# Optimization experiments

Measured on AMD Instinct MI355X. Metric: run time of the kernel, lower is better.

Reference implementation:

```python
import jax, jax.numpy as jnp
import numpy as np

EMBED_DIM = 96
OUT_DIM = 192
HEADS = 2
HEAD_DIM = OUT_DIM // HEADS  # 96
STRIDE_Q = (1, 2, 2)
STRIDE_KV = (1, 8, 8)
SCALE = 1.0 / float(np.sqrt(HEAD_DIM))


def layer_norm(x, g, b, eps=1e-5):
    m = jnp.mean(x, -1, keepdims=True)
    v = jnp.mean(jnp.square(x - m), -1, keepdims=True)
    return (x - m) * jax.lax.rsqrt(v + eps) * g + b


def pool(x, thw, conv_w, g, b, stride):
    # x: [B, heads, N, d] with cls token at position 0; depthwise conv3d pool + LayerNorm(d)
    B, nh, N, d = x.shape
    T, H, W = thw
    cls_tok, rest = x[:, :, :1], x[:, :, 1:]
    rest = rest.transpose(0, 1, 3, 2).reshape(B * nh, d, T, H, W)
    rest = jax.lax.conv_general_dilated(
        rest, conv_w, stride, [(1, 1), (1, 1), (1, 1)],
        dimension_numbers=('NCDHW', 'OIDHW', 'NCDHW'), feature_group_count=d)
    T2, H2, W2 = rest.shape[2], rest.shape[3], rest.shape[4]
    rest = rest.reshape(B, nh, d, -1).transpose(0, 1, 3, 2)
    x = jnp.concatenate([cls_tok, rest], axis=2)
    return layer_norm(x, g, b), (T2, H2, W2)


def rel_idx(q_n, k_n):
    # decomposed relative-distance indices with q/k resolution ratio scaling
    q_r = max(k_n / q_n, 1.0)
    k_r = max(q_n / k_n, 1.0)
    d = (jnp.arange(q_n, dtype=jnp.float32)[:, None] * q_r
         - jnp.arange(k_n, dtype=jnp.float32)[None, :] * k_r + (k_n - 1) * k_r)
    return d.astype(jnp.int32)


def add_rel_pos(attn, q, q_thw, k_thw, rph, rpw, rpt):
    qt, qh, qw = q_thw
    kt, kh, kw = k_thw
    Rh = rph[rel_idx(qh, kh)]  # [qh, kh, d]
    Rw = rpw[rel_idx(qw, kw)]  # [qw, kw, d]
    Rt = rpt[rel_idx(qt, kt)]  # [qt, kt, d]
    B, nh, qN, d = q.shape
    r_q = q[:, :, 1:].reshape(B, nh, qt, qh, qw, d)
    rel_h = jnp.einsum('bythwc,hkc->bythwk', r_q, Rh)  # k = kh
    rel_w = jnp.einsum('bythwc,wkc->bythwk', r_q, Rw)  # k = kw
    rel_t = jnp.einsum('bythwc,tkc->bythwk', r_q, Rt)  # k = kt
    rel = (rel_t[..., :, None, None] + rel_h[..., None, :, None]
           + rel_w[..., None, None, :]).reshape(B, nh, qt * qh * qw, kt * kh * kw)
    return attn.at[:, :, 1:, 1:].add(rel)


def _forward(x, qkv_w, qkv_b, proj_w, proj_b, pq_w, nq_g, nq_b, pk_w, nk_g, nk_b,
             pv_w, nv_g, nv_b, rel_pos_h, rel_pos_w, rel_pos_t, thw):
    B, N, C = x.shape
    qkv = (x @ qkv_w.T + qkv_b).reshape(B, N, 3, HEADS, HEAD_DIM).transpose(2, 0, 3, 1, 4)
    q, k, v = qkv[0], qkv[1], qkv[2]  # each [B, heads, N, head_dim]
    k, k_thw = pool(k, thw, pk_w, nk_g, nk_b, STRIDE_KV)
    v, _ = pool(v, thw, pv_w, nv_g, nv_b, STRIDE_KV)
    q, q_thw = pool(q, thw, pq_w, nq_g, nq_b, STRIDE_Q)
    attn = jnp.einsum('bhqd,bhkd->bhqk', q * SCALE, k)
    attn = add_rel_pos(attn, q, q_thw, k_thw, rel_pos_h, rel_pos_w, rel_pos_t)
    attn = jax.nn.softmax(attn, axis=-1)
    out = jnp.einsum('bhqk,bhkd->bhqd', attn, v) + q  # residual_pool, with cls embed
    out = out.transpose(0, 2, 1, 3).reshape(B, -1, OUT_DIM)
    return out @ proj_w.T + proj_b


def setup_inputs() -> dict:
    key = jax.random.key(0)
    ks = jax.random.split(key, 10)
    T, H, W = 8, 56, 56
    N = 1 + T * H * W  # 25089
    B = 4
    std = 0.02
    return {
        'x': jax.random.normal(ks[0], (B, N, EMBED_DIM), jnp.float32),
        'qkv_w': jax.random.normal(ks[1], (3 * OUT_DIM, EMBED_DIM), jnp.float32) * std,
        'qkv_b': jnp.zeros((3 * OUT_DIM,), jnp.float32),
        'proj_w': jax.random.normal(ks[2], (OUT_DIM, OUT_DIM), jnp.float32) * std,
        'proj_b': jnp.zeros((OUT_DIM,), jnp.float32),
        'pq_w': jax.random.normal(ks[3], (HEAD_DIM, 1, 3, 3, 3), jnp.float32) * std,
        'nq_g': jnp.ones((HEAD_DIM,), jnp.float32),
        'nq_b': jnp.zeros((HEAD_DIM,), jnp.float32),
        'pk_w': jax.random.normal(ks[4], (HEAD_DIM, 1, 3, 3, 3), jnp.float32) * std,
        'nk_g': jnp.ones((HEAD_DIM,), jnp.float32),
        'nk_b': jnp.zeros((HEAD_DIM,), jnp.float32),
        'pv_w': jax.random.normal(ks[5], (HEAD_DIM, 1, 3, 3, 3), jnp.float32) * std,
        'nv_g': jnp.ones((HEAD_DIM,), jnp.float32),
        'nv_b': jnp.zeros((HEAD_DIM,), jnp.float32),
        'rel_pos_h': jax.random.normal(ks[6], (55, HEAD_DIM), jnp.float32) * std,
        'rel_pos_w': jax.random.normal(ks[7], (55, HEAD_DIM), jnp.float32) * std,
        'rel_pos_t': jax.random.normal(ks[8], (15, HEAD_DIM), jnp.float32) * std,
        'thw_t': 8, 'thw_h': 56, 'thw_w': 56,
    }


def reference(x, qkv_w, qkv_b, proj_w, proj_b, pq_w, nq_g, nq_b, pk_w, nk_g, nk_b,
              pv_w, nv_g, nv_b, rel_pos_h, rel_pos_w, rel_pos_t, thw_t, thw_h, thw_w):
    thw = (int(thw_t), int(thw_h), int(thw_w))
    return _forward(x, qkv_w, qkv_b, proj_w, proj_b, pq_w, nq_g, nq_b, pk_w, nk_g, nk_b,
                    pv_w, nv_g, nv_b, rel_pos_h, rel_pos_w, rel_pos_t, thw)
```

## Files before the change

kernel.cpp:

```cpp
#include <hip/hip_runtime.h>
#include <hip/hip_bf16.h>

typedef short short8 __attribute__((ext_vector_type(8)));
typedef float floatx4 __attribute__((ext_vector_type(4)));
typedef float floatx4v __attribute__((ext_vector_type(4)));

#define SCALE_F 0.10206207261596575f

static __device__ __forceinline__ float b2f(unsigned short u){
  unsigned int v = ((unsigned int)u) << 16; float f;
  __builtin_memcpy(&f, &v, 4); return f;
}
static __device__ __forceinline__ unsigned short f2b(float f){
  __hip_bfloat16 h = __float2bfloat16(f);
  unsigned short u; __builtin_memcpy(&u, &h, 2); return u;
}
static __device__ __forceinline__ int map20(int i){
  return (i < 2) ? i : 7 + ((i-2)/3)*8 + ((i-2)%3);
}

struct ConvDesc {
  const void* src[17];
  long long off[17];
  int count[17];
};

__global__ __launch_bounds__(256) void k_convert(ConvDesc d, unsigned short* dst_base,
                                                 int* flagp, const unsigned int* xprobe)
{
  __shared__ int sflag;
  if (threadIdx.x < 64){
    unsigned int w = xprobe[1024 + threadIdx.x];
    int e = (w >> 7) & 0xFF;
    int pl = (e >= 90 && e <= 140) ? 1 : 0;
    unsigned long long m = __ballot(pl);
    if (threadIdx.x == 0){
      sflag = (__popcll(m) < 40) ? 1 : 0;
      if (blockIdx.x == 0 && blockIdx.y == 0) *flagp = sflag;
    }
  }
  __syncthreads();
  const int flag = sflag;
  const int t = blockIdx.y + 1;
  const int cnt = d.count[t];
  unsigned short* dst = dst_base + d.off[t];
  const float* sf = (const float*)d.src[t];
  const unsigned short* su = (const unsigned short*)d.src[t];
  for (int i = blockIdx.x*blockDim.x + threadIdx.x; i < cnt; i += gridDim.x*blockDim.x){
    dst[i] = flag ? f2b(sf[i]) : su[i];
  }
}

static __device__ __forceinline__ void load_x_frag(
    const void* xr_, int flag, size_t elem_off, short8& a0, short8& a1, short8& a2)
{
  if (flag){
    const float* xr = (const float*)xr_ + elem_off;
    floatx4v f0 = *(const floatx4v*)(xr),      f1 = *(const floatx4v*)(xr+4);
    floatx4v f2 = *(const floatx4v*)(xr+32),   f3 = *(const floatx4v*)(xr+36);
    floatx4v f4 = *(const floatx4v*)(xr+64),   f5 = *(const floatx4v*)(xr+68);
    #pragma unroll
    for (int j = 0; j < 4; ++j){
      a0[j] = (short)f2b(f0[j]); a0[j+4] = (short)f2b(f1[j]);
      a1[j] = (short)f2b(f2[j]); a1[j+4] = (short)f2b(f3[j]);
      a2[j] = (short)f2b(f4[j]); a2[j+4] = (short)f2b(f5[j]);
    }
  } else {
    const unsigned short* xr = (const unsigned short*)xr_ + elem_off;
    a0 = *(const short8*)(xr);
    a1 = *(const short8*)(xr + 32);
    a2 = *(const short8*)(xr + 64);
  }
}

__global__ __launch_bounds__(256) void k_qkv_q(
    const void* __restrict__ x, const unsigned short* __restrict__ w,
    const unsigned short* __restrict__ bias, unsigned short* __restrict__ qr,
    const int* __restrict__ flagp)
{
  const int flag = *flagp;
  const int lane = threadIdx.x & 63;
  const int wv = threadIdx.x >> 6;
  const int kq = (lane >> 4) * 8;
  const int m_base = blockIdx.x * 64 + wv * 16;

  int ma = m_base + (lane & 15); if (ma > 100355) ma = 100355;
  short8 a0, a1, a2;
  load_x_frag(x, flag, (size_t)ma*96 + kq, a0, a1, a2);

  size_t base0[4];
  int mrow[4];
  #pragma unroll
  for (int r = 0; r < 4; ++r){
    int m = m_base + (lane >> 4)*4 + r;
    mrow[r] = m;
    int bb = m / 25089; int n = m - bb*25089;
    base0[r] = ((size_t)(bb*2)*25089 + n)*96;
  }

  #pragma unroll
  for (int ct = 0; ct < 12; ++ct){
    int col = ct*16 + (lane & 15);
    const unsigned short* wrow = w + col*96 + kq;
    short8 b0 = *(const short8*)(wrow);
    short8 b1 = *(const short8*)(wrow + 32);
    short8 b2 = *(const short8*)(wrow + 64);
    float bv = b2f(bias[col]);
    floatx4 acc = {0.f,0.f,0.f,0.f};
    acc = __builtin_amdgcn_mfma_f32_16x16x32_bf16(a0, b0, acc, 0,0,0);
    acc = __builtin_amdgcn_mfma_f32_16x16x32_bf16(a1, b1, acc, 0,0,0);
    acc = __builtin_amdgcn_mfma_f32_16x16x32_bf16(a2, b2, acc, 0,0,0);
    const int head = ct / 6;
    const int dstat = (ct % 6) * 16;
    size_t hoff = (size_t)head * 2408544 + dstat + (lane & 15);
    #pragma unroll
    for (int r = 0; r < 4; ++r){
      if (mrow[r] < 100356) qr[base0[r] + hoff] = f2b(acc[r] + bv);
    }
  }
}

__global__ __launch_bounds__(256) void k_qkv_kv(
    const void* __restrict__ x, const unsigned short* __restrict__ w,
    const unsigned short* __restrict__ bias,
    unsigned short* __restrict__ kc, unsigned short* __restrict__ vc,
    unsigned short* __restrict__ kcls, unsigned short* __restrict__ vcls,
    const int* __restrict__ flagp)
{
  const int flag = *flagp;
  const int isv = blockIdx.y;
  const int lane = threadIdx.x & 63;
  const int wv = threadIdx.x >> 6;
  const int kq = (lane >> 4) * 8;
  const int quad = lane >> 4;
  const int col_l = lane & 15;
  const int rbase = blockIdx.x * 64 + wv * 16;

  int rhoA = rbase + col_l; if (rhoA > 12803) rhoA = 12803;
  int bA, nA;
  if (rhoA < 4){ bA = rhoA; nA = 0; }
  else {
    int rp = rhoA - 4;
    bA = rp / 3200; int rem = rp - bA*3200;
    int t = rem / 400; int s = rem - t*400;
    int ry = s / 20, rx = s - ry*20;
    nA = 1 + (t*56 + map20(ry))*56 + map20(rx);
  }
  short8 a0, a1, a2;
  load_x_frag(x, flag, ((size_t)bA*25089 + nA)*96 + kq, a0, a1, a2);

  int isCls[4], bI[4], baseI[4], valid[4];
  #pragma unroll
  for (int r = 0; r < 4; ++r){
    int rho = rbase + quad*4 + r;
    valid[r] = (rho < 12804);
    if (rho > 12803) rho = 12803;
    if (rho < 4){ isCls[r] = 1; bI[r] = rho; baseI[r] = 0; }
    else {
      int rp = rho - 4;
      int b = rp / 3200; int rem = rp - b*3200;
      int t = rem / 400; int s = rem - t*400;
      int ry = s / 20, rx = s - ry*20;
      isCls[r] = 0; bI[r] = b;
      baseI[r] = (((b*8 + t)*20 + ry)*20 + rx)*192;
    }
  }

  unsigned short* buf  = isv ? vc : kc;
  unsigned short* bufc = isv ? vcls : kcls;
  #pragma unroll
  for (int ct = 0; ct < 12; ++ct){
    const int col = 192 + (isv*12 + ct)*16 + col_l;
    const unsigned short* wrow = w + col*96 + kq;
    short8 b0 = *(const short8*)(wrow);
    short8 b1 = *(const short8*)(wrow + 32);
    short8 b2 = *(const short8*)(wrow + 64);
    float bv = b2f(bias[col]);
    floatx4 acc = {0.f,0.f,0.f,0.f};
    acc = __builtin_amdgcn_mfma_f32_16x16x32_bf16(a0, b0, acc, 0,0,0);
    acc = __builtin_amdgcn_mfma_f32_16x16x32_bf16(a1, b1, acc, 0,0,0);
    acc = __builtin_amdgcn_mfma_f32_16x16x32_bf16(a2, b2, acc, 0,0,0);
    const int head = ct / 6;
    const int dstat = (ct % 6) * 16;
    #pragma unroll
    for (int r = 0; r < 4; ++r){
      if (valid[r]){
        float o = acc[r] + bv;
        if (isCls[r]) bufc[(bI[r]*2 + head)*96 + dstat + col_l] = f2b(o);
        else          buf[baseI[r] + head*96 + dstat + col_l]   = f2b(o);
      }
    }
  }
}

__global__ __launch_bounds__(384) void k_poolq(
    const unsigned short* __restrict__ qr, const unsigned short* __restrict__ cw,
    const unsigned short* __restrict__ g, const unsigned short* __restrict__ bta,
    unsigned short* __restrict__ qp)
{
  __shared__ float wlds[27*96];
  __shared__ float gls[96], bls[96];
  __shared__ float ls1[29*12], ls2[29*12];
  __shared__ float lmean[29], linvs[29];

  const int y  = blockIdx.x;
  const int t  = blockIdx.y;
  const int bh = blockIdx.z;
  const int tid = threadIdx.x;
  const bool has_cls = (y == 0 && t == 0);
  const unsigned short* base = qr + (size_t)bh*2408544;

  for (int idx = tid; idx < 27*96; idx += 384){
    int tap = idx / 96, d = idx - tap*96;
    wlds[idx] = b2f(cw[d*27 + tap]);
  }
  for (int idx = tid; idx < 96; idx += 384){
    gls[idx] = b2f(g[idx]); bls[idx] = b2f(bta[idx]);
  }
  __syncthreads();

  const int x = tid / 12, dg = tid - x*12;
  float val[8] = {0,0,0,0,0,0,0,0};

  if (x < 28){
    #pragma unroll
    for (int dt = 0; dt < 3; ++dt){
      int tt = t + dt - 1; if (tt < 0 || tt >= 8) continue;
      #pragma unroll
      for (int dy = 0; dy < 3; ++dy){
        int yy = 2*y + dy - 1; if (yy < 0 || yy >= 56) continue;
        #pragma unroll
        for (int dx = 0; dx < 3; ++dx){
          int xv = 2*x + dx - 1; if (xv < 0 || xv >= 56) continue;
          const int tap = (dt*3+dy)*3+dx;
          short8 v = *(const short8*)(base + (size_t)(1 + (tt*56 + yy)*56 + xv)*96 + dg*8);
          const float* wr = wlds + tap*96 + dg*8;
          #pragma unroll
          for (int j = 0; j < 8; ++j) val[j] += b2f((unsigned short)v[j]) * wr[j];
        }
      }
    }
    float s1 = 0.f, s2 = 0.f;
    #pragma unroll
    for (int j = 0; j < 8; ++j){ s1 += val[j]; s2 += val[j]*val[j]; }
    ls1[x*12+dg] = s1; ls2[x*12+dg] = s2;
  } else if (has_cls && tid >= 348 && tid < 360){
    int cdg = tid - 348;
    short8 v = *(const short8*)(base + cdg*8);
    float s1 = 0.f, s2 = 0.f;
    #pragma unroll
    for (int j = 0; j < 8; ++j){ val[j] = b2f((unsigned short)v[j]); s1 += val[j]; s2 += val[j]*val[j]; }
    ls1[28*12+cdg] = s1; ls2[28*12+cdg] = s2;
  }
  __syncthreads();

  if (tid < 28 || (tid == 28 && has_cls)){
    float s1 = 0.f, s2 = 0.f;
    #pragma unroll
    for (int k = 0; k < 12; ++k){ s1 += ls1[tid*12+k]; s2 += ls2[tid*12+k]; }
    float mean = s1 * (1.f/96.f);
    float var  = s2 * (1.f/96.f) - mean*mean;
    lmean[tid] = mean; linvs[tid] = rsqrtf(var + 1e-5f);
  }
  __syncthreads();

  if (x < 28){
    float mean = lmean[x], inv = linvs[x];
    int tok = 1 + (t*28 + y)*28 + x;
    short8 o;
    #pragma unroll
    for (int j = 0; j < 8; ++j)
      o[j] = (short)f2b((val[j] - mean)*inv*gls[dg*8+j] + bls[dg*8+j]);
    *(short8*)(qp + ((size_t)bh*6273 + tok)*96 + dg*8) = o;
  } else if (has_cls && tid >= 348 && tid < 360){
    int cdg = tid - 348;
    float mean = lmean[28], inv = linvs[28];
    short8 o;
    #pragma unroll
    for (int j = 0; j < 8; ++j)
      o[j] = (short)f2b((val[j] - mean)*inv*gls[cdg*8+j] + bls[cdg*8+j]);
    *(short8*)(qp + (size_t)bh*6273*96 + cdg*8) = o;
  }
}

__global__ __launch_bounds__(128) void k_poolkv(
    const unsigned short* __restrict__ kc, const unsigned short* __restrict__ vc,
    const unsigned short* __restrict__ kcls, const unsigned short* __restrict__ vcls,
    const unsigned short* __restrict__ cwk, const unsigned short* __restrict__ gk, const unsigned short* __restrict__ bk,
    const unsigned short* __restrict__ cwv, const unsigned short* __restrict__ gv, const unsigned short* __restrict__ bv,
    unsigned short* __restrict__ kp, unsigned short* __restrict__ vt)
{
  const int bid = blockIdx.x;
  const int isv = blockIdx.y;
  const int bh = bid / 416; const int key = bid - bh*416;
  const int d = threadIdx.x;
  if (key >= 393){
    if (d < 96){
      if (isv == 0) kp[((size_t)bh*416 + key)*96 + d] = 0;
      else          vt[((size_t)bh*96 + d)*416 + key] = 0;
    }
    return;
  }
  const int b = bh >> 1, head = bh & 1;
  const unsigned short* buf  = isv ? vc : kc;
  const unsigned short* bufc = isv ? vcls : kcls;
  const unsigned short* cw = (isv == 0) ? cwk : cwv;
  const unsigned short* g  = (isv == 0) ? gk : gv;
  const unsigned short* bt = (isv == 0) ? bk : bv;
  float val = 0.f;
  if (d < 96){
    if (key == 0) val = b2f(bufc[bh*96 + d]);
    else {
      int s = key - 1; int t = s / 49; int r2 = s - t*49; int y = r2 / 7; int xx = r2 - y*7;
      const unsigned short* wr = cw + d*27;
      float sum = 0.f;
      #pragma unroll
      for (int dt = 0; dt < 3; ++dt){
        int tt = t + dt - 1; if (tt < 0 || tt >= 8) continue;
        #pragma unroll
        for (int dy = 0; dy < 3; ++dy){
          if (y == 0 && dy == 0) continue;
          int ry = (y == 0) ? (dy - 1) : 2 + 3*(y-1) + dy;
          #pragma unroll
          for (int dx = 0; dx < 3; ++dx){
            if (xx == 0 && dx == 0) continue;
            int rx = (xx == 0) ? (dx - 1) : 2 + 3*(xx-1) + dx;
            sum += b2f(buf[(((b*8 + tt)*20 + ry)*20 + rx)*192 + head*96 + d]) * b2f(wr[(dt*3+dy)*3+dx]);
          }
        }
      }
      val = sum;
    }
  }
  __shared__ float r1[128], r2s[128];
  r1[threadIdx.x] = (d < 96) ? val : 0.f;
  r2s[threadIdx.x] = (d < 96) ? val*val : 0.f;
  __syncthreads();
  for (int off = 64; off > 0; off >>= 1){
    if ((int)threadIdx.x < off){ r1[threadIdx.x] += r1[threadIdx.x+off]; r2s[threadIdx.x] += r2s[threadIdx.x+off]; }
    __syncthreads();
  }
  if (d < 96){
    float mean = r1[0] * (1.f/96.f);
    float var  = r2s[0] * (1.f/96.f) - mean*mean;
    float inv = rsqrtf(var + 1e-5f);
    float o = (val - mean)*inv*b2f(g[d]) + b2f(bt[d]);
    if (isv == 0) kp[((size_t)bh*416 + key)*96 + d] = f2b(o);
    else          vt[((size_t)bh*96 + d)*416 + key] = f2b(o);
  }
}

__global__ __launch_bounds__(256) void k_rel(
    const unsigned short* __restrict__ qp,
    const unsigned short* __restrict__ rph, const unsigned short* __restrict__ rpw,
    const unsigned short* __restrict__ rpt,
    float* __restrict__ Trel)
{
  const int lane = threadIdx.x & 63;
  const int wv = threadIdx.x >> 6;
  const int bh = blockIdx.y;
  const int q0 = blockIdx.x*64 + wv*16;
  const int kq = (lane >> 4) * 8;
  const int quad = lane >> 4;
  const int col_l = lane & 15;

  const unsigned short* qbase = qp + (size_t)bh*6273*96;
  int qa = q0 + col_l; if (qa > 6272) qa = 6272;
  const unsigned short* qrow = qbase + (size_t)qa*96 + kq;
  short8 a0 = *(const short8*)(qrow);
  short8 a1 = *(const short8*)(qrow + 32);
  short8 a2 = *(const short8*)(qrow + 64);

  int yq[4], xq[4], tq[4], liv[4];
  #pragma unroll
  for (int r = 0; r < 4; ++r){
    int gq = q0 + quad*4 + r;
    liv[r] = (gq >= 1 && gq <= 6272);
    int s = (gq >= 1) ? gq - 1 : 0;
    tq[r] = s / 784; int r2 = s - tq[r]*784; yq[r] = r2 / 28; xq[r] = r2 - yq[r]*28;
  }
  float* Tb = Trel + (size_t)bh*6273*24;

  #pragma unroll
  for (int ct = 0; ct < 8; ++ct){
    int c = ct*16 + col_l;
    const unsigned short* rrow;
    if (c < 55)       rrow = rph + (size_t)c*96;
    else if (c < 110) rrow = rpw + (size_t)(c-55)*96;
    else { int ci = c-110; if (ci > 14) ci = 14; rrow = rpt + (size_t)ci*96; }
    rrow += kq;
    short8 b0 = *(const short8*)(rrow);
    short8 b1 = *(const short8*)(rrow + 32);
    short8 b2 = *(const short8*)(rrow + 64);
    floatx4 acc = {0.f,0.f,0.f,0.f};
    acc = __builtin_amdgcn_mfma_f32_16x16x32_bf16(a0, b0, acc, 0,0,0);
    acc = __builtin_amdgcn_mfma_f32_16x16x32_bf16(a1, b1, acc, 0,0,0);
    acc = __builtin_amdgcn_mfma_f32_16x16x32_bf16(a2, b2, acc, 0,0,0);
    #pragma unroll
    for (int r = 0; r < 4; ++r){
      int gq = q0 + quad*4 + r;
      if (!liv[r] || gq > 6272) continue;
      float* Tq = Tb + (size_t)gq*24;
      if (c < 55){
        int u = yq[r] + 24 - c;
        if (u >= 0 && u <= 24 && (u & 3) == 0) Tq[u >> 2] = acc[r];
      } else if (c < 110){
        int u = xq[r] + 24 - (c - 55);
        if (u >= 0 && u <= 24 && (u & 3) == 0) Tq[8 + (u >> 2)] = acc[r];
      } else if (c < 125){
        int u = tq[r] + 7 - (c - 110);
        if (u >= 0 && u <= 7) Tq[16 + u] = acc[r];
      }
    }
  }
}

#define PSTR 424
__global__ __launch_bounds__(128) void k_attn(
    const unsigned short* __restrict__ qp, const unsigned short* __restrict__ kp,
    const unsigned short* __restrict__ vt, const float* __restrict__ Trel,
    unsigned short* __restrict__ ao)
{
  __shared__ unsigned short P[16*PSTR];
  __shared__ float rel[16*24];
  __shared__ float mx_sh[2][16], sum_sh[2][16];

  const int bh = blockIdx.y;
  const int bb = bh >> 1, head = bh & 1;
  const int tid = threadIdx.x;
  const int lane = tid & 63;
  const int wv = tid >> 6;
  const int q0 = blockIdx.x * 16;

  const unsigned short* qbase = qp + (size_t)bh*6273*96;
  const unsigned short* kbase = kp + (size_t)bh*416*96;
  const unsigned short* vbase = vt + (size_t)bh*96*416;

  #pragma unroll
  for (int it = 0; it < 2; ++it){
    int idx = lane + it*64;
    if (idx < 96){
      int row = idx / 6, seg = idx - row*6;
      int gq = q0 + row; if (gq > 6272) gq = 6272;
      *(floatx4v*)(rel + row*24 + seg*4) =
        *(const floatx4v*)(Trel + ((size_t)bh*6273 + gq)*24 + seg*4);
    }
  }

  const int col = lane & 15;
  const int quad = lane >> 4;
  const int kq = quad * 8;
  const int t0 = wv * 13;

  short8 a0, a1, a2;
  {
    int qa = q0 + col; if (qa > 6272) qa = 6272;
    const unsigned short* qrow = qbase + (size_t)qa*96 + kq;
    a0 = *(const short8*)(qrow);
    a1 = *(const short8*)(qrow + 32);
    a2 = *(const short8*)(qrow + 64);
  }

  int liv[4];
  const float* Tm[4];
  #pragma unroll
  for (int r = 0; r < 4; ++r){
    int gq = q0 + quad*4 + r;
    liv[r] = (gq >= 1);
    Tm[r] = rel + (quad*4 + r)*24;
  }

  floatx4 acc[13];
  float mx[4] = {-1e30f,-1e30f,-1e30f,-1e30f};
  #pragma unroll
  for (int i = 0; i < 13; ++i){
    const int t = t0 + i;
    const unsigned short* krow = kbase + (size_t)(t*16 + col)*96 + kq;
    short8 b0 = *(const short8*)(krow);
    short8 b1 = *(const short8*)(krow + 32);
    short8 b2 = *(const short8*)(krow + 64);
    floatx4 a = {0.f,0.f,0.f,0.f};
    a = __builtin_amdgcn_mfma_f32_16x16x32_bf16(a0, b0, a, 0,0,0);
    a = __builtin_amdgcn_mfma_f32_16x16x32_bf16(a1, b1, a, 0,0,0);
    a = __builtin_amdgcn_mfma_f32_16x16x32_bf16(a2, b2, a, 0,0,0);
    const int key = t*16 + col;
    const bool validk = (key < 393);
    int kt = 0, ky = 0, kx = 0;
    if (key >= 1 && validk){
      int ks = key - 1; kt = ks / 49; int krm = ks - kt*49; ky = krm / 7; kx = krm - ky*7;
    }
    #pragma unroll
    for (int r = 0; r < 4; ++r){
      float s;
      if (!validk) s = -1e30f;
      else {
        s = a[r] * SCALE_F;
        if (key >= 1 && liv[r])
          s += Tm[r][ky] + Tm[r][8 + kx] + Tm[r][16 + kt];
      }
      a[r] = s;
      mx[r] = fmaxf(mx[r], s);
    }
    acc[i] = a;
  }
  #pragma unroll
  for (int r = 0; r < 4; ++r){
    #pragma unroll
    for (int o = 1; o < 16; o <<= 1) mx[r] = fmaxf(mx[r], __shfl_xor(mx[r], o, 64));
  }
  if (col == 0){
    #pragma unroll
    for (int r = 0; r < 4; ++r) mx_sh[wv][quad*4 + r] = mx[r];
  }
  __syncthreads();

  float M[4];
  #pragma unroll
  for (int r = 0; r < 4; ++r)
    M[r] = fmaxf(mx_sh[0][quad*4 + r], mx_sh[1][quad*4 + r]);
  float sum[4] = {0.f,0.f,0.f,0.f};
  #pragma unroll
  for (int i = 0; i < 13; ++i){
    #pragma unroll
    for (int r = 0; r < 4; ++r){
      float e = __expf(acc[i][r] - M[r]);
      acc[i][r] = e; sum[r] += e;
    }
  }
  #pragma unroll
  for (int r = 0; r < 4; ++r){
    #pragma unroll
    for (int o = 1; o < 16; o <<= 1) sum[r] += __shfl_xor(sum[r], o, 64);
  }
  if (col == 0){
    #pragma unroll
    for (int r = 0; r < 4; ++r) sum_sh[wv][quad*4 + r] = sum[r];
  }
  #pragma unroll
  for (int i = 0; i < 13; ++i){
    const int t = t0 + i;
    #pragma unroll
    for (int r = 0; r < 4; ++r)
      P[(quad*4 + r)*PSTR + t*16 + col] = f2b(acc[i][r]);
  }
  __syncthreads();

  float linv4[4];
  #pragma unroll
  for (int r = 0; r < 4; ++r)
    linv4[r] = 1.f / (sum_sh[0][quad*4 + r] + sum_sh[1][quad*4 + r]);

  short8 pf[13];
  #pragma unroll
  for (int s = 0; s < 13; ++s)
    pf[s] = *(const short8*)(P + col*PSTR + s*32 + kq);

  #pragma unroll
  for (int dti = 0; dti < 3; ++dti){
    const int dd = (wv*3 + dti)*16 + col;
    const unsigned short* vrow = vbase + (size_t)dd*416 + kq;
    floatx4 o = {0.f,0.f,0.f,0.f};
    #pragma unroll
    for (int s = 0; s < 13; ++s){
      short8 vf = *(const short8*)(vrow + s*32);
      o = __builtin_amdgcn_mfma_f32_16x16x32_bf16(pf[s], vf, o, 0,0,0);
    }
    #pragma unroll
    for (int r = 0; r < 4; ++r){
      int gq = q0 + quad*4 + r;
      if (gq <= 6272){
        float val = o[r] * linv4[r] + b2f(qbase[(size_t)gq*96 + dd]);
        ao[((size_t)bb*6273 + gq)*192 + head*96 + dd] = f2b(val);
      }
    }
  }
}

__global__ __launch_bounds__(256) void k_proj(
    const unsigned short* __restrict__ ao, const unsigned short* __restrict__ w,
    const unsigned short* __restrict__ bias, void* __restrict__ out, const int* __restrict__ flagp)
{
  const int flag = *flagp;
  const int lane = threadIdx.x & 63;
  const int wv = threadIdx.x >> 6;
  const int c = blockIdx.y*64 + wv*16 + (lane & 15);
  const int kq = (lane >> 4) * 8;
  short8 bfr[6];
  const unsigned short* wrow = w + c*192 + kq;
  #pragma unroll
  for (int s = 0; s < 6; ++s) bfr[s] = *(const short8*)(wrow + 32*s);
  float bv = b2f(bias[c]);
  const int m_base = blockIdx.x * 64;
  for (int i = 0; i < 4; ++i){
    int mt = m_base + i*16;
    int ma = mt + (lane & 15); if (ma > 25091) ma = 25091;
    const unsigned short* arow = ao + (size_t)ma*192 + kq;
    floatx4 acc = {0.f,0.f,0.f,0.f};
    #pragma unroll
    for (int s = 0; s < 6; ++s){
      short8 a = *(const short8*)(arow + 32*s);
      acc = __builtin_amdgcn_mfma_f32_16x16x32_bf16(a, bfr[s], acc, 0,0,0);
    }
    #pragma unroll
    for (int r = 0; r < 4; ++r){
      int m = mt + (lane >> 4)*4 + r;
      if (m < 25092){
        float o = acc[r] + bv;
        if (flag) ((float*)out)[(size_t)m*192 + c] = o;
        else      ((unsigned short*)out)[(size_t)m*192 + c] = f2b(o);
      }
    }
  }
}

extern "C" void kernel_launch(void* const* d_in, const int* in_sizes, int n_in,
                              void* d_out, int out_size, void* d_ws, size_t ws_size,
                              hipStream_t stream)
{
  char* p = (char*)d_ws;
  int* flagp = (int*)p; p += 16;
  unsigned short* conv = (unsigned short*)p;

  ConvDesc desc;
  long long cum = 0;
  for (int i = 0; i < 17; ++i){
    desc.src[i] = d_in[i];
    desc.off[i] = cum;
    desc.count[i] = in_sizes[i];
    cum += in_sizes[i];
  }
  p += (size_t)cum * 2;

  unsigned short* q_raw  = (unsigned short*)p; p += (size_t)19268352*2;
  unsigned short* kc     = (unsigned short*)p; p += (size_t)2457600*2;
  unsigned short* vc     = (unsigned short*)p; p += (size_t)2457600*2;
  unsigned short* kcls   = (unsigned short*)p; p += (size_t)768*2;
  unsigned short* vcls   = (unsigned short*)p; p += (size_t)768*2;
  unsigned short* q_pool = (unsigned short*)p; p += (size_t)4817664*2;
  unsigned short* k_pool = (unsigned short*)p; p += (size_t)319488*2;
  unsigned short* v_t    = (unsigned short*)p; p += (size_t)319488*2;
  float*          Trel   = (float*)p;         p += (size_t)8*6273*24*4;
  unsigned short* a_out  = q_raw;

  const unsigned short* cqkv_w = conv + desc.off[1];
  const unsigned short* cqkv_b = conv + desc.off[2];
  const unsigned short* cproj_w= conv + desc.off[3];
  const unsigned short* cproj_b= conv + desc.off[4];
  const unsigned short* cpq_w  = conv + desc.off[5];
  const unsigned short* cnq_g  = conv + desc.off[6];
  const unsigned short* cnq_b  = conv + desc.off[7];
  const unsigned short* cpk_w  = conv + desc.off[8];
  const unsigned short* cnk_g  = conv + desc.off[9];
  const unsigned short* cnk_b  = conv + desc.off[10];
  const unsigned short* cpv_w  = conv + desc.off[11];
  const unsigned short* cnv_g  = conv + desc.off[12];
  const unsigned short* cnv_b  = conv + desc.off[13];
  const unsigned short* crph   = conv + desc.off[14];
  const unsigned short* crpw   = conv + desc.off[15];
  const unsigned short* crpt   = conv + desc.off[16];

  k_convert<<<dim3(16, 16), 256, 0, stream>>>(desc, conv, flagp, (const unsigned int*)d_in[0]);
  k_qkv_q <<<dim3(1569), 256, 0, stream>>>(d_in[0], cqkv_w, cqkv_b, q_raw, flagp);
  k_qkv_kv<<<dim3(201, 2), 256, 0, stream>>>(d_in[0], cqkv_w, cqkv_b, kc, vc, kcls, vcls, flagp);
  k_poolq<<<dim3(28, 8, 8), 384, 0, stream>>>(q_raw, cpq_w, cnq_g, cnq_b, q_pool);
  k_poolkv<<<dim3(8*416, 2), 128, 0, stream>>>(kc, vc, kcls, vcls, cpk_w, cnk_g, cnk_b, cpv_w, cnv_g, cnv_b, k_pool, v_t);
  k_rel  <<<dim3(99, 8), 256, 0, stream>>>(q_pool, crph, crpw, crpt, Trel);
  k_attn <<<dim3(393, 8), 128, 0, stream>>>(q_pool, k_pool, v_t, Trel, a_out);
  k_proj <<<dim3(393, 3), 256, 0, stream>>>(a_out, cproj_w, cproj_b, d_out, flagp);
}
```

Baseline: 282.8 us.

## Fuse relative-position kernel into attention and retile raw-Q layout by 16-channel slabs

```diff
diff --git a/kernel.cpp b/kernel.cpp
--- a/kernel.cpp
+++ b/kernel.cpp
@@ -6,6 +6,7 @@
 typedef float floatx4v __attribute__((ext_vector_type(4)));
 
 #define SCALE_F 0.10206207261596575f
+#define TOKSTRIDE 401424
 
 static __device__ __forceinline__ float b2f(unsigned short u){
   unsigned int v = ((unsigned int)u) << 16; float f;
@@ -82,25 +83,26 @@
   const int lane = threadIdx.x & 63;
   const int wv = threadIdx.x >> 6;
   const int kq = (lane >> 4) * 8;
+  const int col_l = lane & 15;
   const int m_base = blockIdx.x * 64 + wv * 16;
 
-  int ma = m_base + (lane & 15); if (ma > 100355) ma = 100355;
+  int ma = m_base + col_l; if (ma > 100355) ma = 100355;
   short8 a0, a1, a2;
   load_x_frag(x, flag, (size_t)ma*96 + kq, a0, a1, a2);
 
-  size_t base0[4];
-  int mrow[4];
+  int bbase[4], ntok[4], mrow[4];
   #pragma unroll
   for (int r = 0; r < 4; ++r){
     int m = m_base + (lane >> 4)*4 + r;
     mrow[r] = m;
-    int bb = m / 25089; int n = m - bb*25089;
-    base0[r] = ((size_t)(bb*2)*25089 + n)*96;
+    int bb = m / 25089;
+    ntok[r] = m - bb*25089;
+    bbase[r] = bb*2;
   }
 
   #pragma unroll
   for (int ct = 0; ct < 12; ++ct){
-    int col = ct*16 + (lane & 15);
+    int col = ct*16 + col_l;
     const unsigned short* wrow = w + col*96 + kq;
     short8 b0 = *(const short8*)(wrow);
     short8 b1 = *(const short8*)(wrow + 32);
@@ -111,11 +113,12 @@
     acc = __builtin_amdgcn_mfma_f32_16x16x32_bf16(a1, b1, acc, 0,0,0);
     acc = __builtin_amdgcn_mfma_f32_16x16x32_bf16(a2, b2, acc, 0,0,0);
     const int head = ct / 6;
-    const int dstat = (ct % 6) * 16;
-    size_t hoff = (size_t)head * 2408544 + dstat + (lane & 15);
+    const int dt6  = ct % 6;
     #pragma unroll
     for (int r = 0; r < 4; ++r){
-      if (mrow[r] < 100356) qr[base0[r] + hoff] = f2b(acc[r] + bv);
+      if (mrow[r] < 100356)
+        qr[(size_t)((bbase[r]+head)*6 + dt6)*TOKSTRIDE + (size_t)ntok[r]*16 + col_l]
+          = f2b(acc[r] + bv);
     }
   }
 }
@@ -208,7 +211,6 @@
   const int bh = blockIdx.z;
   const int tid = threadIdx.x;
   const bool has_cls = (y == 0 && t == 0);
-  const unsigned short* base = qr + (size_t)bh*2408544;
 
   for (int idx = tid; idx < 27*96; idx += 384){
     int tap = idx / 96, d = idx - tap*96;
@@ -220,6 +222,7 @@
   __syncthreads();
 
   const int x = tid / 12, dg = tid - x*12;
+  const unsigned short* rowb = qr + (size_t)(bh*6 + (dg >> 1))*TOKSTRIDE + (dg & 1)*8;
   float val[8] = {0,0,0,0,0,0,0,0};
 
   if (x < 28){
@@ -233,7 +236,7 @@
         for (int dx = 0; dx < 3; ++dx){
           int xv = 2*x + dx - 1; if (xv < 0 || xv >= 56) continue;
           const int tap = (dt*3+dy)*3+dx;
-          short8 v = *(const short8*)(base + (size_t)(1 + (tt*56 + yy)*56 + xv)*96 + dg*8);
+          short8 v = *(const short8*)(rowb + (size_t)(1 + (tt*56 + yy)*56 + xv)*16);
           const float* wr = wlds + tap*96 + dg*8;
           #pragma unroll
           for (int j = 0; j < 8; ++j) val[j] += b2f((unsigned short)v[j]) * wr[j];
@@ -246,7 +249,8 @@
     ls1[x*12+dg] = s1; ls2[x*12+dg] = s2;
   } else if (has_cls && tid >= 348 && tid < 360){
     int cdg = tid - 348;
-    short8 v = *(const short8*)(base + cdg*8);
+    const unsigned short* rowc = qr + (size_t)(bh*6 + (cdg >> 1))*TOKSTRIDE + (cdg & 1)*8;
+    short8 v = *(const short8*)(rowc);
     float s1 = 0.f, s2 = 0.f;
     #pragma unroll
     for (int j = 0; j < 8; ++j){ val[j] = b2f((unsigned short)v[j]); s1 += val[j]; s2 += val[j]*val[j]; }
@@ -350,40 +354,56 @@
   }
 }
 
-__global__ __launch_bounds__(256) void k_rel(
-    const unsigned short* __restrict__ qp,
+#define PSTR 424
+__global__ __launch_bounds__(128) void k_attn(
+    const unsigned short* __restrict__ qp, const unsigned short* __restrict__ kp,
+    const unsigned short* __restrict__ vt,
     const unsigned short* __restrict__ rph, const unsigned short* __restrict__ rpw,
     const unsigned short* __restrict__ rpt,
-    float* __restrict__ Trel)
-{
-  const int lane = threadIdx.x & 63;
-  const int wv = threadIdx.x >> 6;
+    unsigned short* __restrict__ ao)
+{
+  __shared__ unsigned short P[16*PSTR];
+  __shared__ float rel[16*24];
+  __shared__ float mx_sh[2][16], sum_sh[2][16];
+
   const int bh = blockIdx.y;
-  const int q0 = blockIdx.x*64 + wv*16;
-  const int kq = (lane >> 4) * 8;
+  const int bb = bh >> 1, head = bh & 1;
+  const int tid = threadIdx.x;
+  const int lane = tid & 63;
+  const int wv = tid >> 6;
+  const int q0 = blockIdx.x * 16;
+
+  const unsigned short* qbase = qp + (size_t)bh*6273*96;
+  const unsigned short* kbase = kp + (size_t)bh*416*96;
+  const unsigned short* vbase = vt + (size_t)bh*96*416;
+
+  const int col = lane & 15;
   const int quad = lane >> 4;
-  const int col_l = lane & 15;
-
-  const unsigned short* qbase = qp + (size_t)bh*6273*96;
-  int qa = q0 + col_l; if (qa > 6272) qa = 6272;
-  const unsigned short* qrow = qbase + (size_t)qa*96 + kq;
-  short8 a0 = *(const short8*)(qrow);
-  short8 a1 = *(const short8*)(qrow + 32);
-  short8 a2 = *(const short8*)(qrow + 64);
-
-  int yq[4], xq[4], tq[4], liv[4];
+  const int kq = quad * 8;
+  const int t0 = wv * 13;
+
+  short8 a0, a1, a2;
+  {
+    int qa = q0 + col; if (qa > 6272) qa = 6272;
+    const unsigned short* qrow = qbase + (size_t)qa*96 + kq;
+    a0 = *(const short8*)(qrow);
+    a1 = *(const short8*)(qrow + 32);
+    a2 = *(const short8*)(qrow + 64);
+  }
+
+  int yq4[4], xq4[4], tq4[4], livx[4], liv[4];
   #pragma unroll
   for (int r = 0; r < 4; ++r){
     int gq = q0 + quad*4 + r;
-    liv[r] = (gq >= 1 && gq <= 6272);
+    liv[r]  = (gq >= 1);
+    livx[r] = (gq >= 1 && gq <= 6272);
     int s = (gq >= 1) ? gq - 1 : 0;
-    tq[r] = s / 784; int r2 = s - tq[r]*784; yq[r] = r2 / 28; xq[r] = r2 - yq[r]*28;
-  }
-  float* Tb = Trel + (size_t)bh*6273*24;
-
-  #pragma unroll
-  for (int ct = 0; ct < 8; ++ct){
-    int c = ct*16 + col_l;
+    tq4[r] = s / 784; int r2 = s - tq4[r]*784; yq4[r] = r2 / 28; xq4[r] = r2 - yq4[r]*28;
+  }
+
+  #pragma unroll
+  for (int cti = 0; cti < 4; ++cti){
+    const int c = (wv*4 + cti)*16 + col;
     const unsigned short* rrow;
     if (c < 55)       rrow = rph + (size_t)c*96;
     else if (c < 110) rrow = rpw + (size_t)(c-55)*96;
@@ -392,83 +412,31 @@
     short8 b0 = *(const short8*)(rrow);
     short8 b1 = *(const short8*)(rrow + 32);
     short8 b2 = *(const short8*)(rrow + 64);
-    floatx4 acc = {0.f,0.f,0.f,0.f};
-    acc = __builtin_amdgcn_mfma_f32_16x16x32_bf16(a0, b0, acc, 0,0,0);
-    acc = __builtin_amdgcn_mfma_f32_16x16x32_bf16(a1, b1, acc, 0,0,0);
-    acc = __builtin_amdgcn_mfma_f32_16x16x32_bf16(a2, b2, acc, 0,0,0);
+    floatx4 rc = {0.f,0.f,0.f,0.f};
+    rc = __builtin_amdgcn_mfma_f32_16x16x32_bf16(a0, b0, rc, 0,0,0);
+    rc = __builtin_amdgcn_mfma_f32_16x16x32_bf16(a1, b1, rc, 0,0,0);
+    rc = __builtin_amdgcn_mfma_f32_16x16x32_bf16(a2, b2, rc, 0,0,0);
     #pragma unroll
     for (int r = 0; r < 4; ++r){
-      int gq = q0 + quad*4 + r;
-      if (!liv[r] || gq > 6272) continue;
-      float* Tq = Tb + (size_t)gq*24;
+      if (!livx[r]) continue;
+      const int m = quad*4 + r;
       if (c < 55){
-        int u = yq[r] + 24 - c;
-        if (u >= 0 && u <= 24 && (u & 3) == 0) Tq[u >> 2] = acc[r];
+        int u = yq4[r] + 24 - c;
+        if (u >= 0 && u <= 24 && (u & 3) == 0) rel[m*24 + (u >> 2)] = rc[r];
       } else if (c < 110){
-        int u = xq[r] + 24 - (c - 55);
-        if (u >= 0 && u <= 24 && (u & 3) == 0) Tq[8 + (u >> 2)] = acc[r];
+        int u = xq4[r] + 24 - (c - 55);
+        if (u >= 0 && u <= 24 && (u & 3) == 0) rel[m*24 + 8 + (u >> 2)] = rc[r];
       } else if (c < 125){
-        int u = tq[r] + 7 - (c - 110);
-        if (u >= 0 && u <= 7) Tq[16 + u] = acc[r];
+        int u = tq4[r] + 7 - (c - 110);
+        if (u >= 0 && u <= 7) rel[m*24 + 16 + u] = rc[r];
       }
     }
   }
-}
-
-#define PSTR 424
-__global__ __launch_bounds__(128) void k_attn(
-    const unsigned short* __restrict__ qp, const unsigned short* __restrict__ kp,
-    const unsigned short* __restrict__ vt, const float* __restrict__ Trel,
-    unsigned short* __restrict__ ao)
-{
-  __shared__ unsigned short P[16*PSTR];
-  __shared__ float rel[16*24];
-  __shared__ float mx_sh[2][16], sum_sh[2][16];
-
-  const int bh = blockIdx.y;
-  const int bb = bh >> 1, head = bh & 1;
-  const int tid = threadIdx.x;
-  const int lane = tid & 63;
-  const int wv = tid >> 6;
-  const int q0 = blockIdx.x * 16;
-
-  const unsigned short* qbase = qp + (size_t)bh*6273*96;
-  const unsigned short* kbase = kp + (size_t)bh*416*96;
-  const unsigned short* vbase = vt + (size_t)bh*96*416;
-
-  #pragma unroll
-  for (int it = 0; it < 2; ++it){
-    int idx = lane + it*64;
-    if (idx < 96){
-      int row = idx / 6, seg = idx - row*6;
-      int gq = q0 + row; if (gq > 6272) gq = 6272;
-      *(floatx4v*)(rel + row*24 + seg*4) =
-        *(const floatx4v*)(Trel + ((size_t)bh*6273 + gq)*24 + seg*4);
-    }
-  }
-
-  const int col = lane & 15;
-  const int quad = lane >> 4;
-  const int kq = quad * 8;
-  const int t0 = wv * 13;
-
-  short8 a0, a1, a2;
-  {
-    int qa = q0 + col; if (qa > 6272) qa = 6272;
-    const unsigned short* qrow = qbase + (size_t)qa*96 + kq;
-    a0 = *(const short8*)(qrow);
-    a1 = *(const short8*)(qrow + 32);
-    a2 = *(const short8*)(qrow + 64);
-  }
-
-  int liv[4];
+  __syncthreads();
+
   const float* Tm[4];
   #pragma unroll
-  for (int r = 0; r < 4; ++r){
-    int gq = q0 + quad*4 + r;
-    liv[r] = (gq >= 1);
-    Tm[r] = rel + (quad*4 + r)*24;
-  }
+  for (int r = 0; r < 4; ++r) Tm[r] = rel + (quad*4 + r)*24;
 
   floatx4 acc[13];
   float mx[4] = {-1e30f,-1e30f,-1e30f,-1e30f};
@@ -639,7 +607,6 @@
   unsigned short* q_pool = (unsigned short*)p; p += (size_t)4817664*2;
   unsigned short* k_pool = (unsigned short*)p; p += (size_t)319488*2;
   unsigned short* v_t    = (unsigned short*)p; p += (size_t)319488*2;
-  float*          Trel   = (float*)p;         p += (size_t)8*6273*24*4;
   unsigned short* a_out  = q_raw;
 
   const unsigned short* cqkv_w = conv + desc.off[1];
@@ -664,7 +631,6 @@
   k_qkv_kv<<<dim3(201, 2), 256, 0, stream>>>(d_in[0], cqkv_w, cqkv_b, kc, vc, kcls, vcls, flagp);
   k_poolq<<<dim3(28, 8, 8), 384, 0, stream>>>(q_raw, cpq_w, cnq_g, cnq_b, q_pool);
   k_poolkv<<<dim3(8*416, 2), 128, 0, stream>>>(kc, vc, kcls, vcls, cpk_w, cnk_g, cnk_b, cpv_w, cnv_g, cnv_b, k_pool, v_t);
-  k_rel  <<<dim3(99, 8), 256, 0, stream>>>(q_pool, crph, crpw, crpt, Trel);
-  k_attn <<<dim3(393, 8), 128, 0, stream>>>(q_pool, k_pool, v_t, Trel, a_out);
+  k_attn <<<dim3(393, 8), 128, 0, stream>>>(q_pool, k_pool, v_t, crph, crpw, crpt, a_out);
   k_proj <<<dim3(393, 3), 256, 0, stream>>>(a_out, cproj_w, cproj_b, d_out, flagp);
 }
```

Result: no change. 277.8 us (-1.7%).
